# Optimization experiments

Hardware: AMD Instinct MI355X
Metric: run time of the kernel (lower is better)

Reference implementation:

```python
import jax, jax.numpy as jnp
import numpy as np

B, N, K, H = 4, 1024, 48, 128
E = 128          # edge feature dim; num_in = E + H = 256
FF = 4 * H       # dense feedforward width
EPS = 1e-5
SCALE = 30.0


def gelu(x):
    return jax.nn.gelu(x, approximate=False)


def linear(x, w, b):
    # torch Linear: w is [out, in]
    return x @ w.T + b


def layer_norm(x, g, b):
    mu = jnp.mean(x, axis=-1, keepdims=True)
    var = jnp.var(x, axis=-1, keepdims=True)
    return (x - mu) * jax.lax.rsqrt(var + EPS) * g + b


def gather_nodes(nodes, idx):
    # nodes [B,N,H], idx [B,N,K] -> [B,N,K,H]
    b, n, k = idx.shape
    flat = idx.reshape(b, n * k, 1)
    return jnp.take_along_axis(nodes, flat, axis=1).reshape(b, n, k, -1)


def setup_inputs():
    key = jax.random.key(0)
    ks = jax.random.split(key, 24)
    s = 0.05
    inp = {
        "h_V": jax.random.normal(ks[0], (B, N, H), jnp.float32),
        "h_E": jax.random.normal(ks[1], (B, N, K, E), jnp.float32),
        "E_idx": jax.random.randint(ks[2], (B, N, K), 0, N, jnp.int64),
        "mask_V": jnp.ones((B, N), jnp.float32),
        "mask_attend": jnp.ones((B, N, K), jnp.float32),
        # node-update message MLP (input dim H + E + H = 3H here)
        "W1_w": jax.random.normal(ks[3], (H, H + E + H), jnp.float32) * s,
        "W1_b": jnp.zeros((H,), jnp.float32),
        "W2_w": jax.random.normal(ks[4], (H, H), jnp.float32) * s,
        "W2_b": jnp.zeros((H,), jnp.float32),
        "W3_w": jax.random.normal(ks[5], (H, H), jnp.float32) * s,
        "W3_b": jnp.zeros((H,), jnp.float32),
        # edge-update message MLP
        "W11_w": jax.random.normal(ks[6], (H, H + E + H), jnp.float32) * s,
        "W11_b": jnp.zeros((H,), jnp.float32),
        "W12_w": jax.random.normal(ks[7], (H, H), jnp.float32) * s,
        "W12_b": jnp.zeros((H,), jnp.float32),
        "W13_w": jax.random.normal(ks[8], (H, H), jnp.float32) * s,
        "W13_b": jnp.zeros((H,), jnp.float32),
        # layer norms
        "ln0_g": jnp.ones((H,), jnp.float32), "ln0_b": jnp.zeros((H,), jnp.float32),
        "ln1_g": jnp.ones((H,), jnp.float32), "ln1_b": jnp.zeros((H,), jnp.float32),
        "ln2_g": jnp.ones((H,), jnp.float32), "ln2_b": jnp.zeros((H,), jnp.float32),
        # position-wise feedforward
        "Win_w": jax.random.normal(ks[9], (FF, H), jnp.float32) * s,
        "Win_b": jnp.zeros((FF,), jnp.float32),
        "Wout_w": jax.random.normal(ks[10], (H, FF), jnp.float32) * s,
        "Wout_b": jnp.zeros((H,), jnp.float32),
        # ReZero residual weight (init 0 in the module; nonzero for testing)
        "resweight": jax.random.normal(ks[11], (1,), jnp.float32) * 0.1,
    }
    return inp


def reference(h_V, h_E, E_idx, mask_V, mask_attend,
              W1_w, W1_b, W2_w, W2_b, W3_w, W3_b,
              W11_w, W11_b, W12_w, W12_b, W13_w, W13_b,
              ln0_g, ln0_b, ln1_g, ln1_b, ln2_g, ln2_b,
              Win_w, Win_b, Wout_w, Wout_b, resweight):
    # ---- node update (pre-norm, ReZero-scaled residual), dropout=eval ----
    residual = h_V
    hVn = layer_norm(h_V, ln0_g, ln0_b)
    h_nbr = gather_nodes(hVn, E_idx)                              # [B,N,K,H]
    h_EV = jnp.concatenate(
        [jnp.broadcast_to(hVn[:, :, None, :], (B, N, K, H)), h_E, h_nbr], axis=-1)
    h_message = linear(gelu(linear(gelu(linear(h_EV, W1_w, W1_b)), W2_w, W2_b)), W3_w, W3_b)
    h_message = mask_attend[..., None] * h_message
    dh = jnp.sum(h_message, axis=-2) / SCALE
    h_V = residual + dh * resweight

    # ---- position-wise feedforward ----
    residual = h_V
    hVn = layer_norm(h_V, ln1_g, ln1_b)
    dh = linear(gelu(linear(hVn, Win_w, Win_b)), Wout_w, Wout_b)
    h_V = residual + dh * resweight
    h_V = mask_V[..., None] * h_V

    # ---- edge update (no ReZero scaling on this branch) ----
    residual = h_E
    hEn = layer_norm(h_E, ln2_g, ln2_b)
    h_nbr = gather_nodes(h_V, E_idx)
    h_EV = jnp.concatenate(
        [jnp.broadcast_to(h_V[:, :, None, :], (B, N, K, H)), hEn, h_nbr], axis=-1)
    h_message = linear(gelu(linear(gelu(linear(h_EV, W11_w, W11_b)), W12_w, W12_b)), W13_w, W13_b)
    h_E = residual + h_message

    return h_V, h_E
```

## Files before the change

kernel.cpp:

```cpp
#include <hip/hip_runtime.h>
#include <hip/hip_bf16.h>

#define BB 4
#define NN 1024
#define KK 48
#define HH 128
#define EE 128
#define IN3 384
#define FF 512
#define ST 132

typedef __attribute__((ext_vector_type(8))) short bf16x8;
typedef __attribute__((ext_vector_type(4))) float f32x4;

#define MFMA(a, b, c) __builtin_amdgcn_mfma_f32_16x16x32_bf16((a), (b), (c), 0, 0, 0)

__device__ __forceinline__ float bf2f(ushort u) {
    union { uint i; float f; } v; v.i = ((uint)u) << 16; return v.f;
}
__device__ __forceinline__ uint cvtpk(float a, float b) {
    uint r;
    asm("v_cvt_pk_bf16_f32 %0, %1, %2" : "=v"(r) : "v"(a), "v"(b));
    return r;
}
__device__ __forceinline__ ushort f2bf1(float v) {
    return (ushort)cvtpk(v, v);
}
__device__ __forceinline__ float wsum(float x) {
    #pragma unroll
    for (int o = 32; o; o >>= 1) x += __shfl_xor(x, o, 64);
    return x;
}
__device__ __forceinline__ float gelu_f(float x) {
    float t = x * fmaf(x * x, 0.044715f, 1.0f);
    float a = fminf(t * 2.3022061f, 50.0f);
    float z;
    asm("v_exp_f32 %0, %1" : "=v"(z) : "v"(a));
    float r;
    asm("v_rcp_f32 %0, %1" : "=v"(r) : "v"(z + 1.0f));
    return x * z * r;
}

__global__ __launch_bounds__(256) void k_cvt8(
    const float* __restrict__ s0, const float* __restrict__ s1,
    const float* __restrict__ s2, const float* __restrict__ s3,
    const float* __restrict__ s4, const float* __restrict__ s5,
    const float* __restrict__ s6, const float* __restrict__ s7,
    ushort* __restrict__ d0, ushort* __restrict__ d1,
    ushort* __restrict__ d2, ushort* __restrict__ d3,
    ushort* __restrict__ d4, ushort* __restrict__ d5,
    ushort* __restrict__ d6, ushort* __restrict__ d7) {
    int i = blockIdx.x * 256 + threadIdx.x;
    const float* s; ushort* d; int base;
    if      (i < 12288) { s = s0; d = d0; base = 0; }
    else if (i < 16384) { s = s1; d = d1; base = 12288; }
    else if (i < 20480) { s = s2; d = d2; base = 16384; }
    else if (i < 32768) { s = s3; d = d3; base = 20480; }
    else if (i < 36864) { s = s4; d = d4; base = 32768; }
    else if (i < 40960) { s = s5; d = d5; base = 36864; }
    else if (i < 57344) { s = s6; d = d6; base = 40960; }
    else                { s = s7; d = d7; base = 57344; }
    int j = i - base;
    float4 v = ((const float4*)s)[j];
    uint2 o;
    o.x = cvtpk(v.x, v.y);
    o.y = cvtpk(v.z, v.w);
    ((uint2*)d)[j] = o;
}

__global__ __launch_bounds__(256) void k_ln0(const float* __restrict__ hV,
                                             const float* __restrict__ g,
                                             const float* __restrict__ bta,
                                             ushort* __restrict__ out) {
    int row = blockIdx.x * 4 + (threadIdx.x >> 6);
    int l = threadIdx.x & 63;
    const float* src = hV + (size_t)row * HH;
    float x0 = src[l], x1 = src[l + 64];
    float s = wsum(x0 + x1);
    float q = wsum(x0 * x0 + x1 * x1);
    float mu = s * (1.0f / 128.0f);
    float rstd = rsqrtf(q * (1.0f / 128.0f) - mu * mu + 1e-5f);
    ushort* dst = out + (size_t)row * HH;
    dst[l]      = f2bf1((x0 - mu) * rstd * g[l]      + bta[l]);
    dst[l + 64] = f2bf1((x1 - mu) * rstd * g[l + 64] + bta[l + 64]);
}

__global__ __launch_bounds__(256, 4) void k_node(
    const float* __restrict__ hV, const float* __restrict__ hE,
    const int* __restrict__ Eidx, const float* __restrict__ maskAtt,
    const ushort* __restrict__ W1w, const float* __restrict__ W1b,
    const ushort* __restrict__ W2w, const float* __restrict__ W2b,
    const ushort* __restrict__ W3w, const float* __restrict__ W3b,
    const float* __restrict__ resw,
    const ushort* __restrict__ hVn,
    float* __restrict__ outHVp) {

    __shared__ ushort buf[96 * ST];
    __shared__ float  sMask[96];
    __shared__ float  sCol[256];

    const int t = threadIdx.x;
    const int w = t >> 6;
    const int lane = t & 63;
    const int np = blockIdx.x * 2;
    const int b  = np >> 10;
    const int r16 = lane & 15, g4 = lane >> 4;

    int myidx[6];
    #pragma unroll
    for (int mt = 0; mt < 6; mt++)
        myidx[mt] = Eidx[np * KK + mt * 16 + r16];
    if (t < 96) sMask[t] = maskAtt[np * KK + t];

    f32x4 acc[6][2];
    #pragma unroll
    for (int mt = 0; mt < 6; mt++) {
        acc[mt][0] = (f32x4){0.f, 0.f, 0.f, 0.f};
        acc[mt][1] = (f32x4){0.f, 0.f, 0.f, 0.f};
    }

    const ushort* Wp  = W1w + (w * 32 + r16) * IN3 + g4 * 8;
    const float*  hE0 = hE + (size_t)np * KK * EE;

    #pragma unroll
    for (int kt = 0; kt < 4; kt++) {
        bf16x8 b0 = *(const bf16x8*)(Wp + 128 + kt * 32);
        bf16x8 b1 = *(const bf16x8*)(Wp + 16 * IN3 + 128 + kt * 32);
        #pragma unroll
        for (int mt = 0; mt < 6; mt++) {
            const float* p = hE0 + (size_t)(mt * 16 + r16) * EE + kt * 32 + g4 * 8;
            float4 f0 = *(const float4*)(p);
            float4 f1 = *(const float4*)(p + 4);
            union { uint u[4]; bf16x8 v; } a;
            a.u[0] = cvtpk(f0.x, f0.y); a.u[1] = cvtpk(f0.z, f0.w);
            a.u[2] = cvtpk(f1.x, f1.y); a.u[3] = cvtpk(f1.z, f1.w);
            acc[mt][0] = MFMA(a.v, b0, acc[mt][0]);
            acc[mt][1] = MFMA(a.v, b1, acc[mt][1]);
        }
    }
    {
        const ushort* nb = hVn + (size_t)b * NN * HH + g4 * 8;
        #pragma unroll
        for (int kt = 0; kt < 4; kt++) {
            bf16x8 b0 = *(const bf16x8*)(Wp + 256 + kt * 32);
            bf16x8 b1 = *(const bf16x8*)(Wp + 16 * IN3 + 256 + kt * 32);
            #pragma unroll
            for (int mt = 0; mt < 6; mt++) {
                bf16x8 a = *(const bf16x8*)(nb + (size_t)myidx[mt] * HH + kt * 32);
                acc[mt][0] = MFMA(a, b0, acc[mt][0]);
                acc[mt][1] = MFMA(a, b1, acc[mt][1]);
            }
        }
    }
    {
        const ushort* sp0 = hVn + (size_t)np * HH + g4 * 8;
        const ushort* sp1 = sp0 + HH;
        #pragma unroll
        for (int kt = 0; kt < 4; kt++) {
            bf16x8 a0 = *(const bf16x8*)(sp0 + kt * 32);
            bf16x8 a1 = *(const bf16x8*)(sp1 + kt * 32);
            bf16x8 b0 = *(const bf16x8*)(Wp + kt * 32);
            bf16x8 b1 = *(const bf16x8*)(Wp + 16 * IN3 + kt * 32);
            #pragma unroll
            for (int mt = 0; mt < 6; mt++) {
                bf16x8 a = (mt < 3) ? a0 : a1;
                acc[mt][0] = MFMA(a, b0, acc[mt][0]);
                acc[mt][1] = MFMA(a, b1, acc[mt][1]);
            }
        }
    }
    #pragma unroll
    for (int nn = 0; nn < 2; nn++) {
        int col = w * 32 + nn * 16 + r16;
        float bb = W1b[col];
        #pragma unroll
        for (int mt = 0; mt < 6; mt++)
            #pragma unroll
            for (int r = 0; r < 4; r++)
                buf[(mt * 16 + g4 * 4 + r) * ST + col] = f2bf1(gelu_f(acc[mt][nn][r] + bb));
    }
    __syncthreads();

    f32x4 acc2[6][2];
    #pragma unroll
    for (int mt = 0; mt < 6; mt++) {
        acc2[mt][0] = (f32x4){0.f, 0.f, 0.f, 0.f};
        acc2[mt][1] = (f32x4){0.f, 0.f, 0.f, 0.f};
    }
    {
        const ushort* Wp2 = W2w + (w * 32 + r16) * HH + g4 * 8;
        #pragma unroll
        for (int kt = 0; kt < 4; kt++) {
            bf16x8 b0 = *(const bf16x8*)(Wp2 + kt * 32);
            bf16x8 b1 = *(const bf16x8*)(Wp2 + 16 * HH + kt * 32);
            #pragma unroll
            for (int mt = 0; mt < 6; mt++) {
                bf16x8 a = *(const bf16x8*)&buf[(mt * 16 + r16) * ST + kt * 32 + g4 * 8];
                acc2[mt][0] = MFMA(a, b0, acc2[mt][0]);
                acc2[mt][1] = MFMA(a, b1, acc2[mt][1]);
            }
        }
    }
    __syncthreads();
    #pragma unroll
    for (int nn = 0; nn < 2; nn++) {
        int col = w * 32 + nn * 16 + r16;
        float bb = W2b[col];
        #pragma unroll
        for (int mt = 0; mt < 6; mt++)
            #pragma unroll
            for (int r = 0; r < 4; r++)
                buf[(mt * 16 + g4 * 4 + r) * ST + col] = f2bf1(gelu_f(acc2[mt][nn][r] + bb));
    }
    __syncthreads();

    f32x4 acc3[6][2];
    #pragma unroll
    for (int mt = 0; mt < 6; mt++) {
        acc3[mt][0] = (f32x4){0.f, 0.f, 0.f, 0.f};
        acc3[mt][1] = (f32x4){0.f, 0.f, 0.f, 0.f};
    }
    {
        const ushort* Wp3 = W3w + (w * 32 + r16) * HH + g4 * 8;
        #pragma unroll
        for (int kt = 0; kt < 4; kt++) {
            bf16x8 b0 = *(const bf16x8*)(Wp3 + kt * 32);
            bf16x8 b1 = *(const bf16x8*)(Wp3 + 16 * HH + kt * 32);
            #pragma unroll
            for (int mt = 0; mt < 6; mt++) {
                bf16x8 a = *(const bf16x8*)&buf[(mt * 16 + r16) * ST + kt * 32 + g4 * 8];
                acc3[mt][0] = MFMA(a, b0, acc3[mt][0]);
                acc3[mt][1] = MFMA(a, b1, acc3[mt][1]);
            }
        }
    }
    {
        float b3a = W3b[w * 32 + r16];
        float b3b = W3b[w * 32 + 16 + r16];
        float s0a = 0.f, s0b = 0.f, s1a = 0.f, s1b = 0.f;
        #pragma unroll
        for (int mt = 0; mt < 6; mt++)
            #pragma unroll
            for (int r = 0; r < 4; r++) {
                int row = mt * 16 + g4 * 4 + r;
                float mk = sMask[row];
                float v0 = (acc3[mt][0][r] + b3a) * mk;
                float v1 = (acc3[mt][1][r] + b3b) * mk;
                if (mt < 3) { s0a += v0; s0b += v1; }
                else        { s1a += v0; s1b += v1; }
            }
        s0a += __shfl_xor(s0a, 16, 64); s0a += __shfl_xor(s0a, 32, 64);
        s0b += __shfl_xor(s0b, 16, 64); s0b += __shfl_xor(s0b, 32, 64);
        s1a += __shfl_xor(s1a, 16, 64); s1a += __shfl_xor(s1a, 32, 64);
        s1b += __shfl_xor(s1b, 16, 64); s1b += __shfl_xor(s1b, 32, 64);
        if (g4 == 0) {
            sCol[w * 32 + r16]            = s0a;
            sCol[w * 32 + 16 + r16]       = s0b;
            sCol[128 + w * 32 + r16]      = s1a;
            sCol[128 + w * 32 + 16 + r16] = s1b;
        }
    }
    __syncthreads();

    {
        float rw = resw[0];
        size_t o = (size_t)np * HH + t;
        outHVp[o] = hV[o] + sCol[t] * (1.0f / 30.0f) * rw;
    }
}

__global__ __launch_bounds__(256, 4) void k_ffn(
    const float* __restrict__ maskV,
    const float* __restrict__ ln1g, const float* __restrict__ ln1b,
    const ushort* __restrict__ Winw, const float* __restrict__ Winb,
    const ushort* __restrict__ Woutw, const float* __restrict__ Woutb,
    const float* __restrict__ resw,
    const float* __restrict__ hVp,
    float* __restrict__ outV,
    ushort* __restrict__ hV2b) {

    __shared__ float  sHVp[16 * 132];
    __shared__ ushort sX[16 * 136];
    __shared__ ushort sY[16 * 520];
    __shared__ float  sMk[16];

    const int t = threadIdx.x;
    const int w = t >> 6;
    const int lane = t & 63;
    const int nb = blockIdx.x * 16;
    const int r16 = lane & 15, g4 = lane >> 4;

    #pragma unroll
    for (int i = 0; i < 8; i++) {
        int e = t + i * 256;
        sHVp[(e >> 7) * 132 + (e & 127)] = hVp[(size_t)nb * HH + e];
    }
    if (t < 16) sMk[t] = maskV[nb + t];
    __syncthreads();

    #pragma unroll
    for (int i = 0; i < 4; i++) {
        int row = w * 4 + i;
        float x0 = sHVp[row * 132 + lane], x1 = sHVp[row * 132 + 64 + lane];
        float s = wsum(x0 + x1);
        float q = wsum(x0 * x0 + x1 * x1);
        float mu = s * (1.0f / 128.0f);
        float rstd = rsqrtf(q * (1.0f / 128.0f) - mu * mu + 1e-5f);
        sX[row * 136 + lane]      = f2bf1((x0 - mu) * rstd * ln1g[lane]      + ln1b[lane]);
        sX[row * 136 + 64 + lane] = f2bf1((x1 - mu) * rstd * ln1g[64 + lane] + ln1b[64 + lane]);
    }
    __syncthreads();

    f32x4 acc1[8];
    #pragma unroll
    for (int nn = 0; nn < 8; nn++) acc1[nn] = (f32x4){0.f, 0.f, 0.f, 0.f};
    bf16x8 a1[4];
    #pragma unroll
    for (int kt = 0; kt < 4; kt++)
        a1[kt] = *(const bf16x8*)&sX[r16 * 136 + kt * 32 + g4 * 8];
    #pragma unroll
    for (int nn = 0; nn < 8; nn++) {
        const ushort* Wq = Winw + (w * 128 + nn * 16 + r16) * HH + g4 * 8;
        #pragma unroll
        for (int kt = 0; kt < 4; kt++)
            acc1[nn] = MFMA(a1[kt], *(const bf16x8*)(Wq + kt * 32), acc1[nn]);
    }
    #pragma unroll
    for (int nn = 0; nn < 8; nn++) {
        int col = w * 128 + nn * 16 + r16;
        float bb = Winb[col];
        #pragma unroll
        for (int r = 0; r < 4; r++)
            sY[(g4 * 4 + r) * 520 + col] = f2bf1(gelu_f(acc1[nn][r] + bb));
    }
    __syncthreads();

    f32x4 acc2[2];
    acc2[0] = (f32x4){0.f, 0.f, 0.f, 0.f};
    acc2[1] = (f32x4){0.f, 0.f, 0.f, 0.f};
    {
        const ushort* Wq = Woutw + (w * 32 + r16) * FF + g4 * 8;
        #pragma unroll 4
        for (int kt = 0; kt < 16; kt++) {
            bf16x8 a = *(const bf16x8*)&sY[r16 * 520 + kt * 32 + g4 * 8];
            acc2[0] = MFMA(a, *(const bf16x8*)(Wq + kt * 32), acc2[0]);
            acc2[1] = MFMA(a, *(const bf16x8*)(Wq + 16 * FF + kt * 32), acc2[1]);
        }
    }
    float rw = resw[0];
    #pragma unroll
    for (int nn = 0; nn < 2; nn++) {
        int col = w * 32 + nn * 16 + r16;
        float bb = Woutb[col];
        #pragma unroll
        for (int r = 0; r < 4; r++) {
            int row = g4 * 4 + r;
            float out = sHVp[row * 132 + col] + (acc2[nn][r] + bb) * rw;
            out *= sMk[row];
            outV[(size_t)(nb + row) * HH + col] = out;
            hV2b[(size_t)(nb + row) * HH + col] = f2bf1(out);
        }
    }
}

__global__ __launch_bounds__(256, 4) void k_edge(
    const float* __restrict__ hE, const int* __restrict__ Eidx,
    const ushort* __restrict__ W11w, const float* __restrict__ W11b,
    const ushort* __restrict__ W12w, const float* __restrict__ W12b,
    const ushort* __restrict__ W13w, const float* __restrict__ W13b,
    const float* __restrict__ ln2g, const float* __restrict__ ln2b,
    const ushort* __restrict__ hV2b,
    float* __restrict__ outE) {

    __shared__ ushort buf[96 * ST];

    const int t = threadIdx.x;
    const int w = t >> 6;
    const int lane = t & 63;
    const int np = blockIdx.x * 2;
    const int b  = np >> 10;
    const size_t eb = (size_t)np * KK * EE;
    const int r16 = lane & 15, g4 = lane >> 4;

    int myidx[6];
    #pragma unroll
    for (int mt = 0; mt < 6; mt++)
        myidx[mt] = Eidx[np * KK + mt * 16 + r16];

    {
        float g0 = ln2g[2 * lane], g1 = ln2g[2 * lane + 1];
        float c0 = ln2b[2 * lane], c1 = ln2b[2 * lane + 1];
        #pragma unroll 4
        for (int i = 0; i < 24; i++) {
            int k = w + i * 4;
            float2 pr = ((const float2*)(hE + eb + (size_t)k * EE))[lane];
            float x0 = pr.x, x1 = pr.y;
            float s = wsum(x0 + x1);
            float q = wsum(x0 * x0 + x1 * x1);
            float mu = s * (1.0f / 128.0f);
            float rstd = rsqrtf(q * (1.0f / 128.0f) - mu * mu + 1e-5f);
            uint packed = cvtpk((x0 - mu) * rstd * g0 + c0, (x1 - mu) * rstd * g1 + c1);
            *(uint*)&buf[k * ST + 2 * lane] = packed;
        }
    }
    __syncthreads();

    f32x4 acc[6][2];
    #pragma unroll
    for (int mt = 0; mt < 6; mt++) {
        acc[mt][0] = (f32x4){0.f, 0.f, 0.f, 0.f};
        acc[mt][1] = (f32x4){0.f, 0.f, 0.f, 0.f};
    }
    const ushort* Wp = W11w + (w * 32 + r16) * IN3 + g4 * 8;
    {
        const ushort* nb = hV2b + (size_t)b * NN * HH + g4 * 8;
        #pragma unroll
        for (int kt = 0; kt < 4; kt++) {
            bf16x8 b0 = *(const bf16x8*)(Wp + 256 + kt * 32);
            bf16x8 b1 = *(const bf16x8*)(Wp + 16 * IN3 + 256 + kt * 32);
            #pragma unroll
            for (int mt = 0; mt < 6; mt++) {
                bf16x8 a = *(const bf16x8*)(nb + (size_t)myidx[mt] * HH + kt * 32);
                acc[mt][0] = MFMA(a, b0, acc[mt][0]);
                acc[mt][1] = MFMA(a, b1, acc[mt][1]);
            }
        }
    }
    #pragma unroll
    for (int kt = 0; kt < 4; kt++) {
        bf16x8 b0 = *(const bf16x8*)(Wp + 128 + kt * 32);
        bf16x8 b1 = *(const bf16x8*)(Wp + 16 * IN3 + 128 + kt * 32);
        #pragma unroll
        for (int mt = 0; mt < 6; mt++) {
            bf16x8 a = *(const bf16x8*)&buf[(mt * 16 + r16) * ST + kt * 32 + g4 * 8];
            acc[mt][0] = MFMA(a, b0, acc[mt][0]);
            acc[mt][1] = MFMA(a, b1, acc[mt][1]);
        }
    }
    {
        const ushort* sp0 = hV2b + (size_t)np * HH + g4 * 8;
        const ushort* sp1 = sp0 + HH;
        #pragma unroll
        for (int kt = 0; kt < 4; kt++) {
            bf16x8 a0 = *(const bf16x8*)(sp0 + kt * 32);
            bf16x8 a1s = *(const bf16x8*)(sp1 + kt * 32);
            bf16x8 b0 = *(const bf16x8*)(Wp + kt * 32);
            bf16x8 b1 = *(const bf16x8*)(Wp + 16 * IN3 + kt * 32);
            #pragma unroll
            for (int mt = 0; mt < 6; mt++) {
                bf16x8 a = (mt < 3) ? a0 : a1s;
                acc[mt][0] = MFMA(a, b0, acc[mt][0]);
                acc[mt][1] = MFMA(a, b1, acc[mt][1]);
            }
        }
    }
    __syncthreads();
    #pragma unroll
    for (int nn = 0; nn < 2; nn++) {
        int col = w * 32 + nn * 16 + r16;
        float bb = W11b[col];
        #pragma unroll
        for (int mt = 0; mt < 6; mt++)
            #pragma unroll
            for (int r = 0; r < 4; r++)
                buf[(mt * 16 + g4 * 4 + r) * ST + col] = f2bf1(gelu_f(acc[mt][nn][r] + bb));
    }
    __syncthreads();

    f32x4 acc2[6][2];
    #pragma unroll
    for (int mt = 0; mt < 6; mt++) {
        acc2[mt][0] = (f32x4){0.f, 0.f, 0.f, 0.f};
        acc2[mt][1] = (f32x4){0.f, 0.f, 0.f, 0.f};
    }
    {
        const ushort* Wp2 = W12w + (w * 32 + r16) * HH + g4 * 8;
        #pragma unroll
        for (int kt = 0; kt < 4; kt++) {
            bf16x8 b0 = *(const bf16x8*)(Wp2 + kt * 32);
            bf16x8 b1 = *(const bf16x8*)(Wp2 + 16 * HH + kt * 32);
            #pragma unroll
            for (int mt = 0; mt < 6; mt++) {
                bf16x8 a = *(const bf16x8*)&buf[(mt * 16 + r16) * ST + kt * 32 + g4 * 8];
                acc2[mt][0] = MFMA(a, b0, acc2[mt][0]);
                acc2[mt][1] = MFMA(a, b1, acc2[mt][1]);
            }
        }
    }
    __syncthreads();
    #pragma unroll
    for (int nn = 0; nn < 2; nn++) {
        int col = w * 32 + nn * 16 + r16;
        float bb = W12b[col];
        #pragma unroll
        for (int mt = 0; mt < 6; mt++)
            #pragma unroll
            for (int r = 0; r < 4; r++)
                buf[(mt * 16 + g4 * 4 + r) * ST + col] = f2bf1(gelu_f(acc2[mt][nn][r] + bb));
    }
    __syncthreads();

    f32x4 acc3[6][2];
    #pragma unroll
    for (int mt = 0; mt < 6; mt++) {
        acc3[mt][0] = (f32x4){0.f, 0.f, 0.f, 0.f};
        acc3[mt][1] = (f32x4){0.f, 0.f, 0.f, 0.f};
    }
    {
        const ushort* Wp3 = W13w + (w * 32 + r16) * HH + g4 * 8;
        #pragma unroll
        for (int kt = 0; kt < 4; kt++) {
            bf16x8 b0 = *(const bf16x8*)(Wp3 + kt * 32);
            bf16x8 b1 = *(const bf16x8*)(Wp3 + 16 * HH + kt * 32);
            #pragma unroll
            for (int mt = 0; mt < 6; mt++) {
                bf16x8 a = *(const bf16x8*)&buf[(mt * 16 + r16) * ST + kt * 32 + g4 * 8];
                acc3[mt][0] = MFMA(a, b0, acc3[mt][0]);
                acc3[mt][1] = MFMA(a, b1, acc3[mt][1]);
            }
        }
    }
    #pragma unroll
    for (int nn = 0; nn < 2; nn++) {
        int col = w * 32 + nn * 16 + r16;
        float bb = W13b[col];
        #pragma unroll
        for (int mt = 0; mt < 6; mt++)
            #pragma unroll
            for (int r = 0; r < 4; r++) {
                int row = mt * 16 + g4 * 4 + r;
                size_t off = eb + (size_t)row * EE + col;
                outE[off] = hE[off] + acc3[mt][nn][r] + bb;
            }
    }
}

extern "C" void kernel_launch(void* const* d_in, const int* in_sizes, int n_in,
                              void* d_out, int out_size, void* d_ws, size_t ws_size,
                              hipStream_t stream) {
    const float* hV      = (const float*)d_in[0];
    const float* hE      = (const float*)d_in[1];
    const int*   Eidx    = (const int*)d_in[2];
    const float* maskV   = (const float*)d_in[3];
    const float* maskAtt = (const float*)d_in[4];
    const float* W1w  = (const float*)d_in[5];
    const float* W1b  = (const float*)d_in[6];
    const float* W2w  = (const float*)d_in[7];
    const float* W2b  = (const float*)d_in[8];
    const float* W3w  = (const float*)d_in[9];
    const float* W3b  = (const float*)d_in[10];
    const float* W11w = (const float*)d_in[11];
    const float* W11b = (const float*)d_in[12];
    const float* W12w = (const float*)d_in[13];
    const float* W12b = (const float*)d_in[14];
    const float* W13w = (const float*)d_in[15];
    const float* W13b = (const float*)d_in[16];
    const float* ln0g = (const float*)d_in[17];
    const float* ln0b = (const float*)d_in[18];
    const float* ln1g = (const float*)d_in[19];
    const float* ln1b = (const float*)d_in[20];
    const float* ln2g = (const float*)d_in[21];
    const float* ln2b = (const float*)d_in[22];
    const float* Winw  = (const float*)d_in[23];
    const float* Winb  = (const float*)d_in[24];
    const float* Woutw = (const float*)d_in[25];
    const float* Woutb = (const float*)d_in[26];
    const float* resw  = (const float*)d_in[27];

    float* outV = (float*)d_out;
    float* outE = outV + (size_t)BB * NN * HH;

    char* wsb = (char*)d_ws;
    ushort* wsHVn = (ushort*)wsb;
    float*  wHVp  = (float*)(wsb + (1 << 20));
    ushort* wHV2b = (ushort*)(wsb + 3 * (1 << 20));
    ushort* wW1   = (ushort*)(wsb + 4 * (1 << 20));
    ushort* wW2   = wW1  + HH * IN3;
    ushort* wW3   = wW2  + HH * HH;
    ushort* wW11  = wW3  + HH * HH;
    ushort* wW12  = wW11 + HH * IN3;
    ushort* wW13  = wW12 + HH * HH;
    ushort* wWin  = wW13 + HH * HH;
    ushort* wWout = wWin + FF * HH;

    k_cvt8<<<dim3(288), dim3(256), 0, stream>>>(
        W1w, W2w, W3w, W11w, W12w, W13w, Winw, Woutw,
        wW1, wW2, wW3, wW11, wW12, wW13, wWin, wWout);

    k_ln0<<<dim3(BB * NN / 4), dim3(256), 0, stream>>>(hV, ln0g, ln0b, wsHVn);
    k_node<<<dim3(BB * NN / 2), dim3(256), 0, stream>>>(
        hV, hE, Eidx, maskAtt,
        wW1, W1b, wW2, W2b, wW3, W3b, resw, wsHVn, wHVp);
    k_ffn<<<dim3(BB * NN / 16), dim3(256), 0, stream>>>(
        maskV, ln1g, ln1b, wWin, Winb, wWout, Woutb, resw, wHVp, outV, wHV2b);
    k_edge<<<dim3(BB * NN / 2), dim3(256), 0, stream>>>(
        hE, Eidx, wW11, W11b, wW12, W12b, wW13, W13b,
        ln2g, ln2b, wHV2b, outE);
}
```

Measured before the change: 250.7 us.

## Precompute LN2 and bf16 edge features in separate pass before node/edge kernels

Adds a k_pre kernel that reads h_E once, writing a bf16 copy and a bf16 layer-normed copy into workspace. k_node then reads bf16 edges instead of fp32, and k_edge reads the precomputed LN2 output instead of normalizing in-kernel, which drops one barrier. The intent is to halve edge-feature traffic in the later kernels and move the LN work out of the MFMA kernel. The cost is an extra full pass over h_E plus about 96 MB of bf16 writes, and both paths depend on the workspace being large enough.

```diff
diff --git a/kernel.cpp b/kernel.cpp
--- a/kernel.cpp
+++ b/kernel.cpp
@@ -85,8 +85,31 @@
     dst[l + 64] = f2bf1((x1 - mu) * rstd * g[l + 64] + bta[l + 64]);
 }
 
+__global__ __launch_bounds__(256) void k_pre(const float* __restrict__ hE,
+                                             const float* __restrict__ g,
+                                             const float* __restrict__ bta,
+                                             ushort* __restrict__ heb,
+                                             ushort* __restrict__ ln2o,
+                                             int doHeb) {
+    int row = blockIdx.x * 4 + (threadIdx.x >> 6);
+    int l = threadIdx.x & 63;
+    float2 v = ((const float2*)(hE + (size_t)row * EE))[l];
+    float s = wsum(v.x + v.y);
+    float q = wsum(v.x * v.x + v.y * v.y);
+    float mu = s * (1.0f / 128.0f);
+    float rstd = rsqrtf(q * (1.0f / 128.0f) - mu * mu + 1e-5f);
+    if (doHeb)
+        ((uint*)(heb + (size_t)row * EE))[l] = cvtpk(v.x, v.y);
+    float2 gg = ((const float2*)g)[l];
+    float2 bb = ((const float2*)bta)[l];
+    float y0 = (v.x - mu) * rstd * gg.x + bb.x;
+    float y1 = (v.y - mu) * rstd * gg.y + bb.y;
+    ((uint*)(ln2o + (size_t)row * EE))[l] = cvtpk(y0, y1);
+}
+
 __global__ __launch_bounds__(256, 4) void k_node(
     const float* __restrict__ hV, const float* __restrict__ hE,
+    const ushort* __restrict__ hEb, int useHeb,
     const int* __restrict__ Eidx, const float* __restrict__ maskAtt,
     const ushort* __restrict__ W1w, const float* __restrict__ W1b,
     const ushort* __restrict__ W2w, const float* __restrict__ W2b,
@@ -120,22 +143,37 @@
     }
 
     const ushort* Wp  = W1w + (w * 32 + r16) * IN3 + g4 * 8;
-    const float*  hE0 = hE + (size_t)np * KK * EE;
-
-    #pragma unroll
-    for (int kt = 0; kt < 4; kt++) {
-        bf16x8 b0 = *(const bf16x8*)(Wp + 128 + kt * 32);
-        bf16x8 b1 = *(const bf16x8*)(Wp + 16 * IN3 + 128 + kt * 32);
-        #pragma unroll
-        for (int mt = 0; mt < 6; mt++) {
-            const float* p = hE0 + (size_t)(mt * 16 + r16) * EE + kt * 32 + g4 * 8;
-            float4 f0 = *(const float4*)(p);
-            float4 f1 = *(const float4*)(p + 4);
-            union { uint u[4]; bf16x8 v; } a;
-            a.u[0] = cvtpk(f0.x, f0.y); a.u[1] = cvtpk(f0.z, f0.w);
-            a.u[2] = cvtpk(f1.x, f1.y); a.u[3] = cvtpk(f1.z, f1.w);
-            acc[mt][0] = MFMA(a.v, b0, acc[mt][0]);
-            acc[mt][1] = MFMA(a.v, b1, acc[mt][1]);
+
+    if (useHeb) {
+        const ushort* he0 = hEb + (size_t)np * KK * EE;
+        #pragma unroll
+        for (int kt = 0; kt < 4; kt++) {
+            bf16x8 b0 = *(const bf16x8*)(Wp + 128 + kt * 32);
+            bf16x8 b1 = *(const bf16x8*)(Wp + 16 * IN3 + 128 + kt * 32);
+            #pragma unroll
+            for (int mt = 0; mt < 6; mt++) {
+                bf16x8 a = *(const bf16x8*)(he0 + (size_t)(mt * 16 + r16) * EE + kt * 32 + g4 * 8);
+                acc[mt][0] = MFMA(a, b0, acc[mt][0]);
+                acc[mt][1] = MFMA(a, b1, acc[mt][1]);
+            }
+        }
+    } else {
+        const float* hE0 = hE + (size_t)np * KK * EE;
+        #pragma unroll
+        for (int kt = 0; kt < 4; kt++) {
+            bf16x8 b0 = *(const bf16x8*)(Wp + 128 + kt * 32);
+            bf16x8 b1 = *(const bf16x8*)(Wp + 16 * IN3 + 128 + kt * 32);
+            #pragma unroll
+            for (int mt = 0; mt < 6; mt++) {
+                const float* p = hE0 + (size_t)(mt * 16 + r16) * EE + kt * 32 + g4 * 8;
+                float4 f0 = *(const float4*)(p);
+                float4 f1 = *(const float4*)(p + 4);
+                union { uint u[4]; bf16x8 v; } a;
+                a.u[0] = cvtpk(f0.x, f0.y); a.u[1] = cvtpk(f0.z, f0.w);
+                a.u[2] = cvtpk(f1.x, f1.y); a.u[3] = cvtpk(f1.z, f1.w);
+                acc[mt][0] = MFMA(a.v, b0, acc[mt][0]);
+                acc[mt][1] = MFMA(a.v, b1, acc[mt][1]);
+            }
         }
     }
     {
@@ -365,6 +403,7 @@
 
 __global__ __launch_bounds__(256, 4) void k_edge(
     const float* __restrict__ hE, const int* __restrict__ Eidx,
+    const ushort* __restrict__ ln2pre, int usePre,
     const ushort* __restrict__ W11w, const float* __restrict__ W11b,
     const ushort* __restrict__ W12w, const float* __restrict__ W12b,
     const ushort* __restrict__ W13w, const float* __restrict__ W13b,
@@ -387,7 +426,7 @@
     for (int mt = 0; mt < 6; mt++)
         myidx[mt] = Eidx[np * KK + mt * 16 + r16];
 
-    {
+    if (!usePre) {
         float g0 = ln2g[2 * lane], g1 = ln2g[2 * lane + 1];
         float c0 = ln2b[2 * lane], c1 = ln2b[2 * lane + 1];
         #pragma unroll 4
@@ -402,8 +441,8 @@
             uint packed = cvtpk((x0 - mu) * rstd * g0 + c0, (x1 - mu) * rstd * g1 + c1);
             *(uint*)&buf[k * ST + 2 * lane] = packed;
         }
-    }
-    __syncthreads();
+        __syncthreads();
+    }
 
     f32x4 acc[6][2];
     #pragma unroll
@@ -426,15 +465,30 @@
             }
         }
     }
-    #pragma unroll
-    for (int kt = 0; kt < 4; kt++) {
-        bf16x8 b0 = *(const bf16x8*)(Wp + 128 + kt * 32);
-        bf16x8 b1 = *(const bf16x8*)(Wp + 16 * IN3 + 128 + kt * 32);
-        #pragma unroll
-        for (int mt = 0; mt < 6; mt++) {
-            bf16x8 a = *(const bf16x8*)&buf[(mt * 16 + r16) * ST + kt * 32 + g4 * 8];
-            acc[mt][0] = MFMA(a, b0, acc[mt][0]);
-            acc[mt][1] = MFMA(a, b1, acc[mt][1]);
+    if (usePre) {
+        const ushort* lp = ln2pre + eb;
+        #pragma unroll
+        for (int kt = 0; kt < 4; kt++) {
+            bf16x8 b0 = *(const bf16x8*)(Wp + 128 + kt * 32);
+            bf16x8 b1 = *(const bf16x8*)(Wp + 16 * IN3 + 128 + kt * 32);
+            #pragma unroll
+            for (int mt = 0; mt < 6; mt++) {
+                bf16x8 a = *(const bf16x8*)(lp + (size_t)(mt * 16 + r16) * EE + kt * 32 + g4 * 8);
+                acc[mt][0] = MFMA(a, b0, acc[mt][0]);
+                acc[mt][1] = MFMA(a, b1, acc[mt][1]);
+            }
+        }
+    } else {
+        #pragma unroll
+        for (int kt = 0; kt < 4; kt++) {
+            bf16x8 b0 = *(const bf16x8*)(Wp + 128 + kt * 32);
+            bf16x8 b1 = *(const bf16x8*)(Wp + 16 * IN3 + 128 + kt * 32);
+            #pragma unroll
+            for (int mt = 0; mt < 6; mt++) {
+                bf16x8 a = *(const bf16x8*)&buf[(mt * 16 + r16) * ST + kt * 32 + g4 * 8];
+                acc[mt][0] = MFMA(a, b0, acc[mt][0]);
+                acc[mt][1] = MFMA(a, b1, acc[mt][1]);
+            }
         }
     }
     {
@@ -454,7 +508,7 @@
             }
         }
     }
-    __syncthreads();
+    if (!usePre) __syncthreads();
     #pragma unroll
     for (int nn = 0; nn < 2; nn++) {
         int col = w * 32 + nn * 16 + r16;
@@ -570,11 +624,12 @@
     float* outV = (float*)d_out;
     float* outE = outV + (size_t)BB * NN * HH;
 
+    const size_t MB = 1 << 20;
     char* wsb = (char*)d_ws;
     ushort* wsHVn = (ushort*)wsb;
-    float*  wHVp  = (float*)(wsb + (1 << 20));
-    ushort* wHV2b = (ushort*)(wsb + 3 * (1 << 20));
-    ushort* wW1   = (ushort*)(wsb + 4 * (1 << 20));
+    float*  wHVp  = (float*)(wsb + 1 * MB);
+    ushort* wHV2b = (ushort*)(wsb + 3 * MB);
+    ushort* wW1   = (ushort*)(wsb + 4 * MB);
     ushort* wW2   = wW1  + HH * IN3;
     ushort* wW3   = wW2  + HH * HH;
     ushort* wW11  = wW3  + HH * HH;
@@ -582,18 +637,27 @@
     ushort* wW13  = wW12 + HH * HH;
     ushort* wWin  = wW13 + HH * HH;
     ushort* wWout = wWin + FF * HH;
+    ushort* wLN2  = (ushort*)(wsb + 6 * MB);
+    ushort* wHEb  = (ushort*)(wsb + 54 * MB);
+
+    int usePre = (ws_size >= 54 * MB) ? 1 : 0;
+    int useHeb = (ws_size >= 102 * MB) ? 1 : 0;
 
     k_cvt8<<<dim3(288), dim3(256), 0, stream>>>(
         W1w, W2w, W3w, W11w, W12w, W13w, Winw, Woutw,
         wW1, wW2, wW3, wW11, wW12, wW13, wWin, wWout);
 
     k_ln0<<<dim3(BB * NN / 4), dim3(256), 0, stream>>>(hV, ln0g, ln0b, wsHVn);
+    if (usePre)
+        k_pre<<<dim3(BB * NN * KK / 4), dim3(256), 0, stream>>>(
+            hE, ln2g, ln2b, wHEb, wLN2, useHeb);
+
     k_node<<<dim3(BB * NN / 2), dim3(256), 0, stream>>>(
-        hV, hE, Eidx, maskAtt,
+        hV, hE, wHEb, useHeb, Eidx, maskAtt,
         wW1, W1b, wW2, W2b, wW3, W3b, resw, wsHVn, wHVp);
     k_ffn<<<dim3(BB * NN / 16), dim3(256), 0, stream>>>(
         maskV, ln1g, ln1b, wWin, Winb, wWout, Woutb, resw, wHVp, outV, wHV2b);
     k_edge<<<dim3(BB * NN / 2), dim3(256), 0, stream>>>(
-        hE, Eidx, wW11, W11b, wW12, W12b, wW13, W13b,
+        hE, Eidx, wLN2, usePre, wW11, W11b, wW12, W12b, wW13, W13b,
         ln2g, ln2b, wHV2b, outE);
 }
```

New measurement: 301.1 us. 1.2x slower.

## Widen edge kernel to 512 threads and stage h_E in LDS for residual

Applied to the files above, without the earlier changes.

The edge kernel now runs 8 waves per block, split into two row groups of 48 edges and four column groups, which halves per-wave accumulator state. The raw h_E tile is kept in shared memory as bf16 during layer norm, so the final residual add no longer re-reads h_E from global memory. The message output goes through LDS and is written with coalesced float4 stores. This adds a second LDS buffer, which may lower occupancy, and rounds both the residual and the message to bf16, which reduces output precision.

```diff
diff --git a/kernel.cpp b/kernel.cpp
--- a/kernel.cpp
+++ b/kernel.cpp
@@ -363,7 +363,7 @@
     }
 }
 
-__global__ __launch_bounds__(256, 4) void k_edge(
+__global__ __launch_bounds__(512, 4) void k_edge(
     const float* __restrict__ hE, const int* __restrict__ Eidx,
     const ushort* __restrict__ W11w, const float* __restrict__ W11b,
     const ushort* __restrict__ W12w, const float* __restrict__ W12b,
@@ -373,45 +373,48 @@
     float* __restrict__ outE) {
 
     __shared__ ushort buf[96 * ST];
+    __shared__ ushort rawE[96 * ST];
 
     const int t = threadIdx.x;
     const int w = t >> 6;
     const int lane = t & 63;
+    const int rg = w >> 2;
+    const int cg = w & 3;
     const int np = blockIdx.x * 2;
     const int b  = np >> 10;
     const size_t eb = (size_t)np * KK * EE;
     const int r16 = lane & 15, g4 = lane >> 4;
 
-    int myidx[6];
-    #pragma unroll
-    for (int mt = 0; mt < 6; mt++)
-        myidx[mt] = Eidx[np * KK + mt * 16 + r16];
+    int myidx[3];
+    #pragma unroll
+    for (int mt = 0; mt < 3; mt++)
+        myidx[mt] = Eidx[np * KK + rg * 48 + mt * 16 + r16];
 
     {
         float g0 = ln2g[2 * lane], g1 = ln2g[2 * lane + 1];
         float c0 = ln2b[2 * lane], c1 = ln2b[2 * lane + 1];
-        #pragma unroll 4
-        for (int i = 0; i < 24; i++) {
-            int k = w + i * 4;
+        #pragma unroll 3
+        for (int i = 0; i < 12; i++) {
+            int k = w + i * 8;
             float2 pr = ((const float2*)(hE + eb + (size_t)k * EE))[lane];
-            float x0 = pr.x, x1 = pr.y;
-            float s = wsum(x0 + x1);
-            float q = wsum(x0 * x0 + x1 * x1);
+            *(uint*)&rawE[k * ST + 2 * lane] = cvtpk(pr.x, pr.y);
+            float s = wsum(pr.x + pr.y);
+            float q = wsum(pr.x * pr.x + pr.y * pr.y);
             float mu = s * (1.0f / 128.0f);
             float rstd = rsqrtf(q * (1.0f / 128.0f) - mu * mu + 1e-5f);
-            uint packed = cvtpk((x0 - mu) * rstd * g0 + c0, (x1 - mu) * rstd * g1 + c1);
+            uint packed = cvtpk((pr.x - mu) * rstd * g0 + c0, (pr.y - mu) * rstd * g1 + c1);
             *(uint*)&buf[k * ST + 2 * lane] = packed;
         }
     }
     __syncthreads();
 
-    f32x4 acc[6][2];
-    #pragma unroll
-    for (int mt = 0; mt < 6; mt++) {
+    f32x4 acc[3][2];
+    #pragma unroll
+    for (int mt = 0; mt < 3; mt++) {
         acc[mt][0] = (f32x4){0.f, 0.f, 0.f, 0.f};
         acc[mt][1] = (f32x4){0.f, 0.f, 0.f, 0.f};
     }
-    const ushort* Wp = W11w + (w * 32 + r16) * IN3 + g4 * 8;
+    const ushort* Wp = W11w + (cg * 32 + r16) * IN3 + g4 * 8;
     {
         const ushort* nb = hV2b + (size_t)b * NN * HH + g4 * 8;
         #pragma unroll
@@ -419,7 +422,7 @@
             bf16x8 b0 = *(const bf16x8*)(Wp + 256 + kt * 32);
             bf16x8 b1 = *(const bf16x8*)(Wp + 16 * IN3 + 256 + kt * 32);
             #pragma unroll
-            for (int mt = 0; mt < 6; mt++) {
+            for (int mt = 0; mt < 3; mt++) {
                 bf16x8 a = *(const bf16x8*)(nb + (size_t)myidx[mt] * HH + kt * 32);
                 acc[mt][0] = MFMA(a, b0, acc[mt][0]);
                 acc[mt][1] = MFMA(a, b1, acc[mt][1]);
@@ -431,57 +434,54 @@
         bf16x8 b0 = *(const bf16x8*)(Wp + 128 + kt * 32);
         bf16x8 b1 = *(const bf16x8*)(Wp + 16 * IN3 + 128 + kt * 32);
         #pragma unroll
-        for (int mt = 0; mt < 6; mt++) {
-            bf16x8 a = *(const bf16x8*)&buf[(mt * 16 + r16) * ST + kt * 32 + g4 * 8];
+        for (int mt = 0; mt < 3; mt++) {
+            bf16x8 a = *(const bf16x8*)&buf[(rg * 48 + mt * 16 + r16) * ST + kt * 32 + g4 * 8];
             acc[mt][0] = MFMA(a, b0, acc[mt][0]);
             acc[mt][1] = MFMA(a, b1, acc[mt][1]);
         }
     }
     {
-        const ushort* sp0 = hV2b + (size_t)np * HH + g4 * 8;
-        const ushort* sp1 = sp0 + HH;
-        #pragma unroll
-        for (int kt = 0; kt < 4; kt++) {
-            bf16x8 a0 = *(const bf16x8*)(sp0 + kt * 32);
-            bf16x8 a1s = *(const bf16x8*)(sp1 + kt * 32);
+        const ushort* sp = hV2b + (size_t)(np + rg) * HH + g4 * 8;
+        #pragma unroll
+        for (int kt = 0; kt < 4; kt++) {
+            bf16x8 aself = *(const bf16x8*)(sp + kt * 32);
             bf16x8 b0 = *(const bf16x8*)(Wp + kt * 32);
             bf16x8 b1 = *(const bf16x8*)(Wp + 16 * IN3 + kt * 32);
             #pragma unroll
-            for (int mt = 0; mt < 6; mt++) {
-                bf16x8 a = (mt < 3) ? a0 : a1s;
-                acc[mt][0] = MFMA(a, b0, acc[mt][0]);
-                acc[mt][1] = MFMA(a, b1, acc[mt][1]);
+            for (int mt = 0; mt < 3; mt++) {
+                acc[mt][0] = MFMA(aself, b0, acc[mt][0]);
+                acc[mt][1] = MFMA(aself, b1, acc[mt][1]);
             }
         }
     }
     __syncthreads();
     #pragma unroll
     for (int nn = 0; nn < 2; nn++) {
-        int col = w * 32 + nn * 16 + r16;
+        int col = cg * 32 + nn * 16 + r16;
         float bb = W11b[col];
         #pragma unroll
-        for (int mt = 0; mt < 6; mt++)
+        for (int mt = 0; mt < 3; mt++)
             #pragma unroll
             for (int r = 0; r < 4; r++)
-                buf[(mt * 16 + g4 * 4 + r) * ST + col] = f2bf1(gelu_f(acc[mt][nn][r] + bb));
-    }
-    __syncthreads();
-
-    f32x4 acc2[6][2];
-    #pragma unroll
-    for (int mt = 0; mt < 6; mt++) {
+                buf[(rg * 48 + mt * 16 + g4 * 4 + r) * ST + col] = f2bf1(gelu_f(acc[mt][nn][r] + bb));
+    }
+    __syncthreads();
+
+    f32x4 acc2[3][2];
+    #pragma unroll
+    for (int mt = 0; mt < 3; mt++) {
         acc2[mt][0] = (f32x4){0.f, 0.f, 0.f, 0.f};
         acc2[mt][1] = (f32x4){0.f, 0.f, 0.f, 0.f};
     }
     {
-        const ushort* Wp2 = W12w + (w * 32 + r16) * HH + g4 * 8;
+        const ushort* Wp2 = W12w + (cg * 32 + r16) * HH + g4 * 8;
         #pragma unroll
         for (int kt = 0; kt < 4; kt++) {
             bf16x8 b0 = *(const bf16x8*)(Wp2 + kt * 32);
             bf16x8 b1 = *(const bf16x8*)(Wp2 + 16 * HH + kt * 32);
             #pragma unroll
-            for (int mt = 0; mt < 6; mt++) {
-                bf16x8 a = *(const bf16x8*)&buf[(mt * 16 + r16) * ST + kt * 32 + g4 * 8];
+            for (int mt = 0; mt < 3; mt++) {
+                bf16x8 a = *(const bf16x8*)&buf[(rg * 48 + mt * 16 + r16) * ST + kt * 32 + g4 * 8];
                 acc2[mt][0] = MFMA(a, b0, acc2[mt][0]);
                 acc2[mt][1] = MFMA(a, b1, acc2[mt][1]);
             }
@@ -490,48 +490,64 @@
     __syncthreads();
     #pragma unroll
     for (int nn = 0; nn < 2; nn++) {
-        int col = w * 32 + nn * 16 + r16;
+        int col = cg * 32 + nn * 16 + r16;
         float bb = W12b[col];
         #pragma unroll
-        for (int mt = 0; mt < 6; mt++)
+        for (int mt = 0; mt < 3; mt++)
             #pragma unroll
             for (int r = 0; r < 4; r++)
-                buf[(mt * 16 + g4 * 4 + r) * ST + col] = f2bf1(gelu_f(acc2[mt][nn][r] + bb));
-    }
-    __syncthreads();
-
-    f32x4 acc3[6][2];
-    #pragma unroll
-    for (int mt = 0; mt < 6; mt++) {
+                buf[(rg * 48 + mt * 16 + g4 * 4 + r) * ST + col] = f2bf1(gelu_f(acc2[mt][nn][r] + bb));
+    }
+    __syncthreads();
+
+    f32x4 acc3[3][2];
+    #pragma unroll
+    for (int mt = 0; mt < 3; mt++) {
         acc3[mt][0] = (f32x4){0.f, 0.f, 0.f, 0.f};
         acc3[mt][1] = (f32x4){0.f, 0.f, 0.f, 0.f};
     }
     {
-        const ushort* Wp3 = W13w + (w * 32 + r16) * HH + g4 * 8;
+        const ushort* Wp3 = W13w + (cg * 32 + r16) * HH + g4 * 8;
         #pragma unroll
         for (int kt = 0; kt < 4; kt++) {
             bf16x8 b0 = *(const bf16x8*)(Wp3 + kt * 32);
             bf16x8 b1 = *(const bf16x8*)(Wp3 + 16 * HH + kt * 32);
             #pragma unroll
-            for (int mt = 0; mt < 6; mt++) {
-                bf16x8 a = *(const bf16x8*)&buf[(mt * 16 + r16) * ST + kt * 32 + g4 * 8];
+            for (int mt = 0; mt < 3; mt++) {
+                bf16x8 a = *(const bf16x8*)&buf[(rg * 48 + mt * 16 + r16) * ST + kt * 32 + g4 * 8];
                 acc3[mt][0] = MFMA(a, b0, acc3[mt][0]);
                 acc3[mt][1] = MFMA(a, b1, acc3[mt][1]);
             }
         }
     }
+    __syncthreads();
     #pragma unroll
     for (int nn = 0; nn < 2; nn++) {
-        int col = w * 32 + nn * 16 + r16;
+        int col = cg * 32 + nn * 16 + r16;
         float bb = W13b[col];
         #pragma unroll
-        for (int mt = 0; mt < 6; mt++)
-            #pragma unroll
-            for (int r = 0; r < 4; r++) {
-                int row = mt * 16 + g4 * 4 + r;
-                size_t off = eb + (size_t)row * EE + col;
-                outE[off] = hE[off] + acc3[mt][nn][r] + bb;
-            }
+        for (int mt = 0; mt < 3; mt++)
+            #pragma unroll
+            for (int r = 0; r < 4; r++)
+                buf[(rg * 48 + mt * 16 + g4 * 4 + r) * ST + col] = f2bf1(acc3[mt][nn][r] + bb);
+    }
+    __syncthreads();
+
+    {
+        float4* edst = (float4*)(outE + eb);
+        #pragma unroll
+        for (int i = 0; i < 6; i++) {
+            int c = t + i * 512;
+            int k = c >> 5, cp = (c & 31) * 4;
+            const ushort* er = &rawE[k * ST + cp];
+            const ushort* mr = &buf[k * ST + cp];
+            float4 ov;
+            ov.x = bf2f(er[0]) + bf2f(mr[0]);
+            ov.y = bf2f(er[1]) + bf2f(mr[1]);
+            ov.z = bf2f(er[2]) + bf2f(mr[2]);
+            ov.w = bf2f(er[3]) + bf2f(mr[3]);
+            edst[c] = ov;
+        }
     }
 }
 
@@ -570,11 +586,12 @@
     float* outV = (float*)d_out;
     float* outE = outV + (size_t)BB * NN * HH;
 
+    const size_t MB = 1 << 20;
     char* wsb = (char*)d_ws;
     ushort* wsHVn = (ushort*)wsb;
-    float*  wHVp  = (float*)(wsb + (1 << 20));
-    ushort* wHV2b = (ushort*)(wsb + 3 * (1 << 20));
-    ushort* wW1   = (ushort*)(wsb + 4 * (1 << 20));
+    float*  wHVp  = (float*)(wsb + 1 * MB);
+    ushort* wHV2b = (ushort*)(wsb + 3 * MB);
+    ushort* wW1   = (ushort*)(wsb + 4 * MB);
     ushort* wW2   = wW1  + HH * IN3;
     ushort* wW3   = wW2  + HH * HH;
     ushort* wW11  = wW3  + HH * HH;
@@ -593,7 +610,7 @@
         wW1, W1b, wW2, W2b, wW3, W3b, resw, wsHVn, wHVp);
     k_ffn<<<dim3(BB * NN / 16), dim3(256), 0, stream>>>(
         maskV, ln1g, ln1b, wWin, Winb, wWout, Woutb, resw, wHVp, outV, wHV2b);
-    k_edge<<<dim3(BB * NN / 2), dim3(256), 0, stream>>>(
+    k_edge<<<dim3(BB * NN / 2), dim3(512), 0, stream>>>(
         hE, Eidx, wW11, W11b, wW12, W12b, wW13, W13b,
         ln2g, ln2b, wHV2b, outE);
 }
```

Result: slower. 268.7 us (+7.2%).
